# Performance work log

Hardware: AMD Instinct MI355X
Metric: run time of the kernel (lower is better)

The kernel has to match this reference:

```python
import jax, jax.numpy as jnp
import numpy as np

LAMBDA_ATTENTION = 0.33
LAMBDA_DISTANCE = 0.33
LAMBDA_ADJACENCY = 1.0 - LAMBDA_ATTENTION - LAMBDA_DISTANCE
EPS = 1e-06
NEG_INF = 1000000000000.0


def setup_inputs() -> dict:
    key = jax.random.key(0)
    kq, kk, kv, ka, kd = jax.random.split(key, 5)
    B, H, S, D = 16, 16, 512, 64
    return {
        "query": jax.random.normal(kq, (B, H, S, D), dtype=jnp.float32),
        "key": jax.random.normal(kk, (B, H, S, D), dtype=jnp.float32),
        "value": jax.random.normal(kv, (B, H, S, D), dtype=jnp.float32),
        "mask": jnp.ones((B, 1, S), dtype=jnp.float32),
        "adj_matrix": jax.random.uniform(ka, (B, S, S), dtype=jnp.float32),
        "distance_matrix": jax.random.uniform(kd, (B, S, S), dtype=jnp.float32),
    }


def reference(query, key, value, mask, adj_matrix, distance_matrix):
    d_k = query.shape[-1]
    # scores: [B,H,S,S]
    scores = jnp.einsum("bhqd,bhkd->bhqk", query, key) / jnp.sqrt(jnp.asarray(d_k, query.dtype))
    # mask [B,1,S] -> broadcast to [B,H,S,S] over key axis
    key_mask = mask[:, :, None, :]  # [B,1,1,S]
    scores = jnp.where(key_mask == 0, -NEG_INF, scores)
    p_attn = jax.nn.softmax(scores, axis=-1)

    # row-normalized adjacency, broadcast over heads
    adj_norm = adj_matrix / (jnp.sum(adj_matrix, axis=-1, keepdims=True) + EPS)  # [B,S,S]

    # distance kernel: mask key positions with +inf then softmax(-x)
    dist = jnp.where(mask == 0, jnp.inf, distance_matrix)  # mask [B,1,S] broadcasts over rows
    p_dist = jax.nn.softmax(-dist, axis=-1)  # [B,S,S]

    p_weighted = (LAMBDA_ATTENTION * p_attn
                  + LAMBDA_DISTANCE * p_dist[:, None, :, :]
                  + LAMBDA_ADJACENCY * adj_norm[:, None, :, :])
    # dropout is identity in eval mode
    out = jnp.einsum("bhqk,bhkd->bhqd", p_weighted, value)
    return out, p_attn
```

## Files before the change

kernel.cpp:

```cpp
#include <hip/hip_runtime.h>
#include <cmath>

#define BATCH 16
#define HEADS 16
#define SEQ   512
#define DIM   64
#define QT    32
#define NCHUNK 8

#define LAMBDA_A 0.33f
#define LAMBDA_D 0.33f
#define LAMBDA_J 0.34f
#define NEG_BIG  1.0e12f

typedef float  floatx4 __attribute__((ext_vector_type(4)));
typedef short  shortx8 __attribute__((ext_vector_type(8)));
typedef short  shortx4 __attribute__((ext_vector_type(4)));

__device__ __forceinline__ unsigned short f2bf(float x){
  unsigned u = __builtin_bit_cast(unsigned, x);
  u += 0x7FFFu + ((u >> 16) & 1u);
  return (unsigned short)(u >> 16);
}

__global__ __launch_bounds__(256, 4) void attn_kernel(
    const float* __restrict__ Q, const float* __restrict__ K, const float* __restrict__ V,
    const float* __restrict__ mask, const float* __restrict__ adj, const float* __restrict__ dist,
    float* __restrict__ out, float* __restrict__ pattn){

  int bx  = blockIdx.x;
  int h   = bx & 15;
  int rest= bx >> 4;
  int qt  = rest & 15;
  int b   = rest >> 4;
  int bh  = b * HEADS + h;
  int q0  = qt * QT;

  int tid  = threadIdx.x;
  int wave = tid >> 6;
  int lane = tid & 63;
  int l15  = lane & 15;
  int quad = lane >> 4;

  __shared__ short sQ [32 * 72];
  __shared__ short sKV[64 * 72];
  __shared__ short sPW[32 * 72];
  __shared__ float sMask[SEQ];
  __shared__ float sRedM[2][32];
  __shared__ float sRedS[2][32];
  __shared__ float sRowA[32];
  __shared__ float sRowD[32];

  const float* Qb = Q + ((size_t)bh * SEQ + q0) * DIM;
  const float* Kb = K + (size_t)bh * SEQ * DIM;
  const float* Vb = V + (size_t)bh * SEQ * DIM;

#pragma unroll
  for (int i = 0; i < 2; i++){
    int f = i * 1024 + tid * 4;
    floatx4 v = *(const floatx4*)(Qb + f);
    int row = f >> 6, col = f & 63;
    shortx4 hh;
    hh[0] = (short)f2bf(v[0] * 0.125f);
    hh[1] = (short)f2bf(v[1] * 0.125f);
    hh[2] = (short)f2bf(v[2] * 0.125f);
    hh[3] = (short)f2bf(v[3] * 0.125f);
    *(shortx4*)&sQ[row * 72 + col] = hh;
  }
  sMask[tid]       = mask[b * SEQ + tid];
  sMask[tid + 256] = mask[b * SEQ + tid + 256];
  __syncthreads();

  {
    int rl  = tid >> 3;
    int sub = tid & 7;
    const float* arow = adj  + ((size_t)b * SEQ + q0 + rl) * SEQ;
    const float* drow = dist + ((size_t)b * SEQ + q0 + rl) * SEQ;
    float asum = 0.f, dsum = 0.f;
#pragma unroll
    for (int k = 0; k < 16; k++){
      int c4 = (k * 8 + sub) * 4;
      floatx4 a4 = *(const floatx4*)(arow + c4);
      floatx4 d4 = *(const floatx4*)(drow + c4);
      asum += (a4[0] + a4[1]) + (a4[2] + a4[3]);
#pragma unroll
      for (int i = 0; i < 4; i++){
        float mk = sMask[c4 + i];
        dsum += (mk == 0.f) ? 0.f : __expf(-d4[i]);
      }
    }
#pragma unroll
    for (int off = 1; off < 8; off <<= 1){
      asum += __shfl_xor(asum, off);
      dsum += __shfl_xor(dsum, off);
    }
    if (sub == 0){
      sRowA[rl] = 1.f / (asum + 1e-6f);
      sRowD[rl] = 1.f / dsum;
    }
  }

  int mtile = wave & 1;
  int p     = wave >> 1;

  floatx4 acc[16];
#pragma unroll
  for (int j = 0; j < 16; j++) acc[j] = (floatx4)0.f;

  for (int c = 0; c < NCHUNK; c++){
    if (c) __syncthreads();
    const float* Kc = Kb + c * 64 * DIM;
#pragma unroll
    for (int i = 0; i < 4; i++){
      int f = i * 1024 + tid * 4;
      floatx4 v = *(const floatx4*)(Kc + f);
      int row = f >> 6, col = f & 63;
      shortx4 hh;
      hh[0] = (short)f2bf(v[0]);
      hh[1] = (short)f2bf(v[1]);
      hh[2] = (short)f2bf(v[2]);
      hh[3] = (short)f2bf(v[3]);
      *(shortx4*)&sKV[row * 72 + col] = hh;
    }
    __syncthreads();
#pragma unroll
    for (int ks = 0; ks < 2; ks++){
      shortx8 af = *(const shortx8*)&sQ[(mtile * 16 + l15) * 72 + ks * 32 + quad * 8];
      shortx8 b0 = *(const shortx8*)&sKV[(p * 16 + l15) * 72 + ks * 32 + quad * 8];
      acc[2 * c] = __builtin_amdgcn_mfma_f32_16x16x32_bf16(af, b0, acc[2 * c], 0, 0, 0);
      shortx8 b1 = *(const shortx8*)&sKV[((p + 2) * 16 + l15) * 72 + ks * 32 + quad * 8];
      acc[2 * c + 1] = __builtin_amdgcn_mfma_f32_16x16x32_bf16(af, b1, acc[2 * c + 1], 0, 0, 0);
    }
  }

  float vmax[4] = {-INFINITY, -INFINITY, -INFINITY, -INFINITY};
#pragma unroll
  for (int j = 0; j < 16; j++){
    int n = (2 * j + p) * 16 + l15;
    bool msk0 = (sMask[n] == 0.f);
#pragma unroll
    for (int r = 0; r < 4; r++){
      float s = msk0 ? -NEG_BIG : acc[j][r];
      acc[j][r] = s;
      vmax[r] = fmaxf(vmax[r], s);
    }
  }
#pragma unroll
  for (int r = 0; r < 4; r++){
#pragma unroll
    for (int off = 1; off < 16; off <<= 1)
      vmax[r] = fmaxf(vmax[r], __shfl_xor(vmax[r], off));
  }
  if (l15 == 0){
#pragma unroll
    for (int r = 0; r < 4; r++) sRedM[p][mtile * 16 + quad * 4 + r] = vmax[r];
  }
  __syncthreads();
  float mrow[4];
#pragma unroll
  for (int r = 0; r < 4; r++){
    int ridx = mtile * 16 + quad * 4 + r;
    mrow[r] = fmaxf(sRedM[0][ridx], sRedM[1][ridx]);
  }
  float vsum[4] = {0.f, 0.f, 0.f, 0.f};
#pragma unroll
  for (int j = 0; j < 16; j++){
#pragma unroll
    for (int r = 0; r < 4; r++){
      float e = __expf(acc[j][r] - mrow[r]);
      acc[j][r] = e;
      vsum[r] += e;
    }
  }
#pragma unroll
  for (int r = 0; r < 4; r++){
#pragma unroll
    for (int off = 1; off < 16; off <<= 1)
      vsum[r] += __shfl_xor(vsum[r], off);
  }
  if (l15 == 0){
#pragma unroll
    for (int r = 0; r < 4; r++) sRedS[p][mtile * 16 + quad * 4 + r] = vsum[r];
  }
  __syncthreads();
  float inv_l[4];
#pragma unroll
  for (int r = 0; r < 4; r++){
    int ridx = mtile * 16 + quad * 4 + r;
    inv_l[r] = 1.f / (sRedS[0][ridx] + sRedS[1][ridx]);
  }

  float* pA = pattn + ((size_t)bh * SEQ + q0) * SEQ;
  const float* arow_base = adj  + ((size_t)b * SEQ + q0) * SEQ;
  const float* drow_base = dist + ((size_t)b * SEQ + q0) * SEQ;

  floatx4 acc2[2];
  acc2[0] = (floatx4)0.f;
  acc2[1] = (floatx4)0.f;

  for (int c = 0; c < NCHUNK; c++){
    if (c) __syncthreads();
    {
      int n = tid & 63, g = tid >> 6;
      const float* Vc = Vb + c * 64 * DIM;
      shortx8 w0, w1;
#pragma unroll
      for (int i = 0; i < 8; i++)  w0[i] = (short)f2bf(Vc[(g * 16 + i) * DIM + n]);
#pragma unroll
      for (int i = 0; i < 8; i++)  w1[i] = (short)f2bf(Vc[(g * 16 + 8 + i) * DIM + n]);
      *(shortx8*)&sKV[n * 72 + g * 16]     = w0;
      *(shortx8*)&sKV[n * 72 + g * 16 + 8] = w1;
    }
#pragma unroll
    for (int r = 0; r < 4; r++){
      int rl = mtile * 16 + quad * 4 + r;
      float ia = sRowA[rl];
      float il = sRowD[rl];
#pragma unroll
      for (int jj = 0; jj < 2; jj++){
        int nloc = (2 * jj + p) * 16 + l15;
        int n    = c * 64 + nloc;
        float pa = acc[2 * c + jj][r] * inv_l[r];
        __builtin_nontemporal_store(pa, &pA[(size_t)rl * SEQ + n]);
        float a  = arow_base[(size_t)rl * SEQ + n];
        float dd = drow_base[(size_t)rl * SEQ + n];
        float mk = sMask[n];
        float pd = (mk == 0.f) ? 0.f : __expf(-dd) * il;
        float pw = LAMBDA_A * pa + LAMBDA_D * pd + LAMBDA_J * a * ia;
        sPW[rl * 72 + nloc] = (short)f2bf(pw);
      }
    }
    __syncthreads();
#pragma unroll
    for (int ks = 0; ks < 2; ks++){
      shortx8 af = *(const shortx8*)&sPW[(mtile * 16 + l15) * 72 + ks * 32 + quad * 8];
      shortx8 b0 = *(const shortx8*)&sKV[(p * 16 + l15) * 72 + ks * 32 + quad * 8];
      acc2[0] = __builtin_amdgcn_mfma_f32_16x16x32_bf16(af, b0, acc2[0], 0, 0, 0);
      shortx8 b1 = *(const shortx8*)&sKV[((p + 2) * 16 + l15) * 72 + ks * 32 + quad * 8];
      acc2[1] = __builtin_amdgcn_mfma_f32_16x16x32_bf16(af, b1, acc2[1], 0, 0, 0);
    }
  }

  float* ob = out + ((size_t)bh * SEQ + q0) * DIM;
#pragma unroll
  for (int t = 0; t < 2; t++){
    int nt = p + 2 * t;
#pragma unroll
    for (int r = 0; r < 4; r++){
      int rl = mtile * 16 + quad * 4 + r;
      __builtin_nontemporal_store(acc2[t][r], &ob[(size_t)rl * DIM + nt * 16 + l15]);
    }
  }
}

extern "C" void kernel_launch(void* const* d_in, const int* in_sizes, int n_in,
                              void* d_out, int out_size, void* d_ws, size_t ws_size,
                              hipStream_t stream){
  const float* Q    = (const float*)d_in[0];
  const float* K    = (const float*)d_in[1];
  const float* V    = (const float*)d_in[2];
  const float* mask = (const float*)d_in[3];
  const float* adj  = (const float*)d_in[4];
  const float* dist = (const float*)d_in[5];
  float* out   = (float*)d_out;
  float* pattn = out + (size_t)BATCH * HEADS * SEQ * DIM;

  attn_kernel<<<BATCH * HEADS * (SEQ / QT), 256, 0, stream>>>(Q, K, V, mask, adj, dist,
                                                              out, pattn);
}
```

Before: 567.3 us.

## Precompute head-invariant adjacency/distance weights and bf16 K/V^T in prep kernels

Adds a prep kernel that computes the combined, normalized adjacency and distance weight matrix once per batch instead of once per head. A second prep kernel converts K to bf16 and writes a transposed bf16 V into workspace. The attention kernel then reads MFMA operands directly from global memory, keeps Q in registers, and double-buffers the probability tile in shared memory. This removes 16x redundant adj/dist reads and exp work plus the per-chunk LDS staging and barriers, at the cost of two extra launches and workspace traffic.

```diff
diff --git a/kernel.cpp b/kernel.cpp
--- a/kernel.cpp
+++ b/kernel.cpp
@@ -23,11 +23,104 @@
   return (unsigned short)(u >> 16);
 }
 
+__global__ __launch_bounds__(256, 8) void prep_w_kernel(
+    const float* __restrict__ adj, const float* __restrict__ dist,
+    const float* __restrict__ mask, float* __restrict__ W)
+{
+  int tid  = threadIdx.x;
+  int lane = tid & 63;
+  int row  = blockIdx.x * 4 + (tid >> 6);
+  int b = row >> 9, q = row & (SEQ - 1);
+  const float* arow = adj  + ((size_t)b * SEQ + q) * SEQ;
+  const float* drow = dist + ((size_t)b * SEQ + q) * SEQ;
+  const float* mrow = mask + (size_t)b * SEQ;
+
+  floatx4 a[2], e[2];
+  float asum = 0.f, dsum = 0.f;
+#pragma unroll
+  for (int i = 0; i < 2; i++){
+    int c4 = (i * 64 + lane) * 4;
+    a[i] = *(const floatx4*)(arow + c4);
+    floatx4 d4 = *(const floatx4*)(drow + c4);
+    floatx4 m4 = *(const floatx4*)(mrow + c4);
+#pragma unroll
+    for (int j = 0; j < 4; j++){
+      asum += a[i][j];
+      float ex = (m4[j] == 0.f) ? 0.f : __expf(-d4[j]);
+      e[i][j] = ex;
+      dsum += ex;
+    }
+  }
+#pragma unroll
+  for (int off = 1; off < 64; off <<= 1){
+    asum += __shfl_xor(asum, off);
+    dsum += __shfl_xor(dsum, off);
+  }
+  float ia = LAMBDA_J / (asum + 1e-6f);
+  float id = LAMBDA_D / dsum;
+
+  float* wrow = W + ((size_t)b * SEQ + q) * SEQ;
+#pragma unroll
+  for (int i = 0; i < 2; i++){
+    int c4 = (i * 64 + lane) * 4;
+    floatx4 w;
+#pragma unroll
+    for (int j = 0; j < 4; j++) w[j] = e[i][j] * id + a[i][j] * ia;
+    *(floatx4*)(wrow + c4) = w;
+  }
+}
+
+__global__ __launch_bounds__(256, 8) void prep_kvt_kernel(
+    const float* __restrict__ K, const float* __restrict__ V,
+    unsigned short* __restrict__ Kb, unsigned short* __restrict__ VTb)
+{
+  int tid = threadIdx.x;
+  int c   = blockIdx.x & 7;
+  int bh  = blockIdx.x >> 3;
+  const float* Kp = K + ((size_t)bh * SEQ + c * 64) * DIM;
+  const float* Vp = V + ((size_t)bh * SEQ + c * 64) * DIM;
+  unsigned short* Ko = Kb  + ((size_t)bh * SEQ + c * 64) * DIM;
+  unsigned short* Vo = VTb + (size_t)bh * DIM * SEQ;
+
+  __shared__ unsigned short sT[64 * 72];
+
+#pragma unroll
+  for (int i = 0; i < 2; i++){
+    int idx = (i * 256 + tid) * 8;
+    floatx4 v0 = *(const floatx4*)(Kp + idx);
+    floatx4 v1 = *(const floatx4*)(Kp + idx + 4);
+    shortx8 hh;
+#pragma unroll
+    for (int j = 0; j < 4; j++){
+      hh[j]     = (short)f2bf(v0[j]);
+      hh[j + 4] = (short)f2bf(v1[j]);
+    }
+    *(shortx8*)(Ko + idx) = hh;
+  }
+
+#pragma unroll
+  for (int i = 0; i < 4; i++){
+    int idx = (i * 256 + tid) * 4;
+    int k = idx >> 6, d = idx & 63;
+    floatx4 v = *(const floatx4*)(Vp + idx);
+#pragma unroll
+    for (int j = 0; j < 4; j++) sT[(d + j) * 72 + k] = f2bf(v[j]);
+  }
+  __syncthreads();
+#pragma unroll
+  for (int i = 0; i < 2; i++){
+    int idx = i * 256 + tid;
+    int d = idx >> 3, k8 = idx & 7;
+    shortx8 hh = *(const shortx8*)&sT[d * 72 + k8 * 8];
+    *(shortx8*)(Vo + (size_t)d * SEQ + c * 64 + k8 * 8) = hh;
+  }
+}
+
 __global__ __launch_bounds__(256, 4) void attn_kernel(
-    const float* __restrict__ Q, const float* __restrict__ K, const float* __restrict__ V,
-    const float* __restrict__ mask, const float* __restrict__ adj, const float* __restrict__ dist,
-    float* __restrict__ out, float* __restrict__ pattn){
-
+    const float* __restrict__ Q, const unsigned short* __restrict__ Kb,
+    const unsigned short* __restrict__ VTb, const float* __restrict__ mask,
+    const float* __restrict__ W, float* __restrict__ out, float* __restrict__ pattn)
+{
   int bx  = blockIdx.x;
   int h   = bx & 15;
   int rest= bx >> 4;
@@ -41,95 +134,46 @@
   int lane = tid & 63;
   int l15  = lane & 15;
   int quad = lane >> 4;
-
-  __shared__ short sQ [32 * 72];
-  __shared__ short sKV[64 * 72];
-  __shared__ short sPW[32 * 72];
+  int mtile = wave & 1;
+  int p     = wave >> 1;
+
   __shared__ float sMask[SEQ];
+  __shared__ unsigned short sPW[2][32 * 72];
   __shared__ float sRedM[2][32];
   __shared__ float sRedS[2][32];
-  __shared__ float sRowA[32];
-  __shared__ float sRowD[32];
-
-  const float* Qb = Q + ((size_t)bh * SEQ + q0) * DIM;
-  const float* Kb = K + (size_t)bh * SEQ * DIM;
-  const float* Vb = V + (size_t)bh * SEQ * DIM;
-
-#pragma unroll
-  for (int i = 0; i < 2; i++){
-    int f = i * 1024 + tid * 4;
-    floatx4 v = *(const floatx4*)(Qb + f);
-    int row = f >> 6, col = f & 63;
-    shortx4 hh;
-    hh[0] = (short)f2bf(v[0] * 0.125f);
-    hh[1] = (short)f2bf(v[1] * 0.125f);
-    hh[2] = (short)f2bf(v[2] * 0.125f);
-    hh[3] = (short)f2bf(v[3] * 0.125f);
-    *(shortx4*)&sQ[row * 72 + col] = hh;
-  }
+
   sMask[tid]       = mask[b * SEQ + tid];
   sMask[tid + 256] = mask[b * SEQ + tid + 256];
+
+  const float* Qb = Q + ((size_t)bh * SEQ + q0 + mtile * 16 + l15) * DIM;
+  shortx8 af[2];
+#pragma unroll
+  for (int ks = 0; ks < 2; ks++){
+    const float* qp = Qb + ks * 32 + quad * 8;
+    floatx4 v0 = *(const floatx4*)qp;
+    floatx4 v1 = *(const floatx4*)(qp + 4);
+#pragma unroll
+    for (int j = 0; j < 4; j++){
+      af[ks][j]     = (short)f2bf(v0[j] * 0.125f);
+      af[ks][j + 4] = (short)f2bf(v1[j] * 0.125f);
+    }
+  }
   __syncthreads();
 
-  {
-    int rl  = tid >> 3;
-    int sub = tid & 7;
-    const float* arow = adj  + ((size_t)b * SEQ + q0 + rl) * SEQ;
-    const float* drow = dist + ((size_t)b * SEQ + q0 + rl) * SEQ;
-    float asum = 0.f, dsum = 0.f;
-#pragma unroll
-    for (int k = 0; k < 16; k++){
-      int c4 = (k * 8 + sub) * 4;
-      floatx4 a4 = *(const floatx4*)(arow + c4);
-      floatx4 d4 = *(const floatx4*)(drow + c4);
-      asum += (a4[0] + a4[1]) + (a4[2] + a4[3]);
-#pragma unroll
-      for (int i = 0; i < 4; i++){
-        float mk = sMask[c4 + i];
-        dsum += (mk == 0.f) ? 0.f : __expf(-d4[i]);
-      }
-    }
-#pragma unroll
-    for (int off = 1; off < 8; off <<= 1){
-      asum += __shfl_xor(asum, off);
-      dsum += __shfl_xor(dsum, off);
-    }
-    if (sub == 0){
-      sRowA[rl] = 1.f / (asum + 1e-6f);
-      sRowD[rl] = 1.f / dsum;
-    }
-  }
-
-  int mtile = wave & 1;
-  int p     = wave >> 1;
-
+  const unsigned short* Kw = Kb + (size_t)bh * SEQ * DIM
+                               + (size_t)(p * 16 + l15) * DIM + quad * 8;
   floatx4 acc[16];
 #pragma unroll
   for (int j = 0; j < 16; j++) acc[j] = (floatx4)0.f;
-
-  for (int c = 0; c < NCHUNK; c++){
-    if (c) __syncthreads();
-    const float* Kc = Kb + c * 64 * DIM;
-#pragma unroll
-    for (int i = 0; i < 4; i++){
-      int f = i * 1024 + tid * 4;
-      floatx4 v = *(const floatx4*)(Kc + f);
-      int row = f >> 6, col = f & 63;
-      shortx4 hh;
-      hh[0] = (short)f2bf(v[0]);
-      hh[1] = (short)f2bf(v[1]);
-      hh[2] = (short)f2bf(v[2]);
-      hh[3] = (short)f2bf(v[3]);
-      *(shortx4*)&sKV[row * 72 + col] = hh;
-    }
-    __syncthreads();
+#pragma unroll
+  for (int cc = 0; cc < NCHUNK; cc++){
+    const unsigned short* Kc = Kw + cc * 64 * DIM;
 #pragma unroll
     for (int ks = 0; ks < 2; ks++){
-      shortx8 af = *(const shortx8*)&sQ[(mtile * 16 + l15) * 72 + ks * 32 + quad * 8];
-      shortx8 b0 = *(const shortx8*)&sKV[(p * 16 + l15) * 72 + ks * 32 + quad * 8];
-      acc[2 * c] = __builtin_amdgcn_mfma_f32_16x16x32_bf16(af, b0, acc[2 * c], 0, 0, 0);
-      shortx8 b1 = *(const shortx8*)&sKV[((p + 2) * 16 + l15) * 72 + ks * 32 + quad * 8];
-      acc[2 * c + 1] = __builtin_amdgcn_mfma_f32_16x16x32_bf16(af, b1, acc[2 * c + 1], 0, 0, 0);
+      shortx8 b0 = *(const shortx8*)(Kc + ks * 32);
+      acc[2 * cc]     = __builtin_amdgcn_mfma_f32_16x16x32_bf16(af[ks], b0, acc[2 * cc], 0, 0, 0);
+      shortx8 b1 = *(const shortx8*)(Kc + 32 * DIM + ks * 32);
+      acc[2 * cc + 1] = __builtin_amdgcn_mfma_f32_16x16x32_bf16(af[ks], b1, acc[2 * cc + 1], 0, 0, 0);
     }
   }
 
@@ -191,53 +235,63 @@
   }
 
   float* pA = pattn + ((size_t)bh * SEQ + q0) * SEQ;
-  const float* arow_base = adj  + ((size_t)b * SEQ + q0) * SEQ;
-  const float* drow_base = dist + ((size_t)b * SEQ + q0) * SEQ;
+  const float* Wq = W + ((size_t)b * SEQ + q0) * SEQ;
+  const unsigned short* Vw = VTb + (size_t)bh * DIM * SEQ
+                                 + (size_t)(p * 16 + l15) * SEQ + quad * 8;
 
   floatx4 acc2[2];
   acc2[0] = (floatx4)0.f;
   acc2[1] = (floatx4)0.f;
 
-  for (int c = 0; c < NCHUNK; c++){
-    if (c) __syncthreads();
-    {
-      int n = tid & 63, g = tid >> 6;
-      const float* Vc = Vb + c * 64 * DIM;
-      shortx8 w0, w1;
-#pragma unroll
-      for (int i = 0; i < 8; i++)  w0[i] = (short)f2bf(Vc[(g * 16 + i) * DIM + n]);
-#pragma unroll
-      for (int i = 0; i < 8; i++)  w1[i] = (short)f2bf(Vc[(g * 16 + 8 + i) * DIM + n]);
-      *(shortx8*)&sKV[n * 72 + g * 16]     = w0;
-      *(shortx8*)&sKV[n * 72 + g * 16 + 8] = w1;
+  float wreg[4][2];
+#pragma unroll
+  for (int r = 0; r < 4; r++){
+    int rl = mtile * 16 + quad * 4 + r;
+#pragma unroll
+    for (int jj = 0; jj < 2; jj++){
+      int nloc = (2 * jj + p) * 16 + l15;
+      wreg[r][jj] = Wq[(size_t)rl * SEQ + nloc];
+    }
+  }
+
+#pragma unroll
+  for (int cc = 0; cc < NCHUNK; cc++){
+    int buf = cc & 1;
+    shortx8 vt0[2], vt1[2];
+#pragma unroll
+    for (int ks = 0; ks < 2; ks++){
+      vt0[ks] = *(const shortx8*)(Vw + cc * 64 + ks * 32);
+      vt1[ks] = *(const shortx8*)(Vw + (size_t)32 * SEQ + cc * 64 + ks * 32);
     }
 #pragma unroll
     for (int r = 0; r < 4; r++){
       int rl = mtile * 16 + quad * 4 + r;
-      float ia = sRowA[rl];
-      float il = sRowD[rl];
 #pragma unroll
       for (int jj = 0; jj < 2; jj++){
         int nloc = (2 * jj + p) * 16 + l15;
-        int n    = c * 64 + nloc;
-        float pa = acc[2 * c + jj][r] * inv_l[r];
+        int n    = cc * 64 + nloc;
+        float pa = acc[2 * cc + jj][r] * inv_l[r];
         __builtin_nontemporal_store(pa, &pA[(size_t)rl * SEQ + n]);
-        float a  = arow_base[(size_t)rl * SEQ + n];
-        float dd = drow_base[(size_t)rl * SEQ + n];
-        float mk = sMask[n];
-        float pd = (mk == 0.f) ? 0.f : __expf(-dd) * il;
-        float pw = LAMBDA_A * pa + LAMBDA_D * pd + LAMBDA_J * a * ia;
-        sPW[rl * 72 + nloc] = (short)f2bf(pw);
+        float pw = LAMBDA_A * pa + wreg[r][jj];
+        sPW[buf][rl * 72 + nloc] = f2bf(pw);
       }
     }
+    int cn = (cc + 1) & 7;
+#pragma unroll
+    for (int r = 0; r < 4; r++){
+      int rl = mtile * 16 + quad * 4 + r;
+#pragma unroll
+      for (int jj = 0; jj < 2; jj++){
+        int nloc = (2 * jj + p) * 16 + l15;
+        wreg[r][jj] = Wq[(size_t)rl * SEQ + cn * 64 + nloc];
+      }
+    }
     __syncthreads();
 #pragma unroll
     for (int ks = 0; ks < 2; ks++){
-      shortx8 af = *(const shortx8*)&sPW[(mtile * 16 + l15) * 72 + ks * 32 + quad * 8];
-      shortx8 b0 = *(const shortx8*)&sKV[(p * 16 + l15) * 72 + ks * 32 + quad * 8];
-      acc2[0] = __builtin_amdgcn_mfma_f32_16x16x32_bf16(af, b0, acc2[0], 0, 0, 0);
-      shortx8 b1 = *(const shortx8*)&sKV[((p + 2) * 16 + l15) * 72 + ks * 32 + quad * 8];
-      acc2[1] = __builtin_amdgcn_mfma_f32_16x16x32_bf16(af, b1, acc2[1], 0, 0, 0);
+      shortx8 a2 = *(const shortx8*)&sPW[buf][(mtile * 16 + l15) * 72 + ks * 32 + quad * 8];
+      acc2[0] = __builtin_amdgcn_mfma_f32_16x16x32_bf16(a2, vt0[ks], acc2[0], 0, 0, 0);
+      acc2[1] = __builtin_amdgcn_mfma_f32_16x16x32_bf16(a2, vt1[ks], acc2[1], 0, 0, 0);
     }
   }
 
@@ -265,6 +319,12 @@
   float* out   = (float*)d_out;
   float* pattn = out + (size_t)BATCH * HEADS * SEQ * DIM;
 
-  attn_kernel<<<BATCH * HEADS * (SEQ / QT), 256, 0, stream>>>(Q, K, V, mask, adj, dist,
-                                                              out, pattn);
-}
+  float*          Wbuf = (float*)d_ws;
+  unsigned short* Kb   = (unsigned short*)((char*)d_ws + (size_t)16 * 1024 * 1024);
+  unsigned short* VTb  = (unsigned short*)((char*)d_ws + (size_t)32 * 1024 * 1024);
+
+  prep_w_kernel  <<<BATCH * SEQ / 4,            256, 0, stream>>>(adj, dist, mask, Wbuf);
+  prep_kvt_kernel<<<BATCH * HEADS * NCHUNK,     256, 0, stream>>>(K, V, Kb, VTb);
+  attn_kernel    <<<BATCH * HEADS * (SEQ / QT), 256, 0, stream>>>(Q, Kb, VTb, mask, Wbuf,
+                                                                  out, pattn);
+}
```

After: 510.3 us. 1.11x faster.
